# Kernel tuning notes

Hardware: AMD Instinct MI355X
Metric: run time of the kernel (lower is better)

Reference implementation:

```python
import jax, jax.numpy as jnp
import numpy as np

HEADS = 4
OUT = 64  # hidden_channels


def gat_conv(x, src, dst, N, W, att_src, att_dst, bias):
    # x: [N, Fin] -> h: [N, H, C]
    h = (x @ W).reshape(N, HEADS, OUT)
    a_s = (h * att_src).sum(-1)  # [N, H]
    a_d = (h * att_dst).sum(-1)  # [N, H]
    logits = jax.nn.leaky_relu(a_s[src] + a_d[dst], negative_slope=0.2)  # [E, H]
    # segment softmax over incoming edges of each destination node
    m = jax.ops.segment_max(logits, dst, num_segments=N)
    e = jnp.exp(logits - m[dst])
    z = jax.ops.segment_sum(e, dst, num_segments=N)
    alpha = e / (z[dst] + 1e-16)
    out = jax.ops.segment_sum(h[src] * alpha[:, :, None], dst, num_segments=N)
    return out.reshape(N, HEADS * OUT) + bias


def setup_inputs() -> dict:
    key = jax.random.key(0)
    ks = jax.random.split(key, 16)
    N, E, F = 50000, 800000, 128
    HC = HEADS * OUT  # 256
    s = 0.1
    return {
        "x": jax.random.normal(ks[0], (N, F), jnp.float32),
        "edge_index": jax.random.randint(ks[1], (2, E), 0, N, dtype=jnp.int32),
        "W1": jax.random.normal(ks[2], (F, HC), jnp.float32) * s,
        "as1": jax.random.normal(ks[3], (1, HEADS, OUT), jnp.float32) * s,
        "ad1": jax.random.normal(ks[4], (1, HEADS, OUT), jnp.float32) * s,
        "b1": jnp.zeros((HC,), jnp.float32),
        "W2": jax.random.normal(ks[5], (HC, HC), jnp.float32) * s,
        "as2": jax.random.normal(ks[6], (1, HEADS, OUT), jnp.float32) * s,
        "ad2": jax.random.normal(ks[7], (1, HEADS, OUT), jnp.float32) * s,
        "b2": jnp.zeros((HC,), jnp.float32),
        "lw1": jax.random.normal(ks[8], (HC, OUT), jnp.float32) * s,
        "lb1": jnp.zeros((OUT,), jnp.float32),
        "lw2": jax.random.normal(ks[9], (OUT, 2), jnp.float32) * s,
        "lb2": jnp.zeros((2,), jnp.float32),
    }


def reference(x, edge_index, W1, as1, ad1, b1, W2, as2, ad2, b2, lw1, lb1, lw2, lb2):
    N = x.shape[0]
    # PyG GATConv default add_self_loops=True
    loop = jnp.arange(N, dtype=edge_index.dtype)
    src = jnp.concatenate([edge_index[0], loop])
    dst = jnp.concatenate([edge_index[1], loop])
    h = jax.nn.elu(gat_conv(x, src, dst, N, W1, as1, ad1, b1))
    # dropout is identity at inference
    h = jax.nn.elu(gat_conv(h, src, dst, N, W2, as2, ad2, b2))
    h = jax.nn.relu(h @ lw1 + lb1)
    return jax.nn.log_softmax(h @ lw2 + lb2, axis=1)
```

## Files before the change

### kernel.cpp

```cpp
#include <hip/hip_runtime.h>
#include <math.h>


typedef __attribute__((ext_vector_type(8))) _Float16 half8v;
typedef __attribute__((ext_vector_type(4))) float f32x4;

__device__ __forceinline__ float lrelu(float x) { return x > 0.f ? x : 0.2f * x; }
__device__ __forceinline__ float elu1(float x) { return x > 0.f ? x : (__expf(x) - 1.f); }

__global__ void convert_x_kernel(const float* __restrict__ src, _Float16* __restrict__ dst,
                                 long n) {
  long i = ((long)blockIdx.x * blockDim.x + threadIdx.x) * 8;
  if (i >= n) return;
  float4 a = *(const float4*)(src + i);
  float4 b = *(const float4*)(src + i + 4);
  half8v o = {(_Float16)a.x, (_Float16)a.y, (_Float16)a.z, (_Float16)a.w,
              (_Float16)b.x, (_Float16)b.y, (_Float16)b.z, (_Float16)b.w};
  *(half8v*)(dst + i) = o;
}

__global__ void convert_weights_kernel(const float* __restrict__ W1, const float* __restrict__ W2,
                                       const float* __restrict__ lw1,
                                       _Float16* __restrict__ o1, _Float16* __restrict__ o2,
                                       _Float16* __restrict__ o3) {
  int t = blockIdx.x * blockDim.x + threadIdx.x;
  if (t < 32768) {
    int n = t >> 7, k = t & 127;
    o1[t] = (_Float16)W1[(long)k * 256 + n];
  } else if (t < 98304) {
    int i = t - 32768;
    int n = i >> 8, k = i & 255;
    o2[i] = (_Float16)W2[(long)k * 256 + n];
  } else if (t < 114688) {
    int i = t - 98304;
    int n = i >> 8, k = i & 255;
    o3[i] = (_Float16)lw1[(long)k * 64 + n];
  }
}

__global__ void zero_int_kernel(int* __restrict__ p, int n) {
  int i = blockIdx.x * blockDim.x + threadIdx.x;
  if (i < n) p[i] = 0;
}

__global__ void count_kernel(const int* __restrict__ dst, int E, int* __restrict__ indeg) {
  int e = blockIdx.x * blockDim.x + threadIdx.x;
  if (e < E) atomicAdd(&indeg[dst[e]], 1);
}

__global__ void scan_block_kernel(const int* __restrict__ in, int* __restrict__ incl,
                                  int* __restrict__ bsum, int N) {
  __shared__ int wsum[16];
  int gid = blockIdx.x * 1024 + threadIdx.x;
  int lane = threadIdx.x & 63, w = threadIdx.x >> 6;
  int v = (gid < N) ? in[gid] : 0;
  int sv = v;
#pragma unroll
  for (int o = 1; o < 64; o <<= 1) {
    int t = __shfl_up(sv, o);
    if (lane >= o) sv += t;
  }
  if (lane == 63) wsum[w] = sv;
  __syncthreads();
  if (w == 0) {
    int bs = (lane < 16) ? wsum[lane] : 0;
#pragma unroll
    for (int o = 1; o < 16; o <<= 1) {
      int t = __shfl_up(bs, o);
      if (lane >= o) bs += t;
    }
    if (lane < 16) wsum[lane] = bs;
  }
  __syncthreads();
  if (w > 0) sv += wsum[w - 1];
  if (gid < N) incl[gid] = sv;
  if (threadIdx.x == 1023) bsum[blockIdx.x] = sv;
}

__global__ void scan_tops_kernel(int* __restrict__ bsum, int nb) {
  int lane = threadIdx.x;
  int v = (lane < nb) ? bsum[lane] : 0;
#pragma unroll
  for (int o = 1; o < 64; o <<= 1) {
    int t = __shfl_up(v, o);
    if (lane >= o) v += t;
  }
  if (lane < nb) bsum[lane] = v;
}

__global__ void scan_finalize_kernel(const int* __restrict__ in, const int* __restrict__ incl,
                                     const int* __restrict__ bsum, int* __restrict__ off,
                                     int* __restrict__ cursor, int N) {
  int gid = blockIdx.x * blockDim.x + threadIdx.x;
  if (gid >= N) return;
  int b = gid >> 10;
  int ic = incl[gid] + ((b > 0) ? bsum[b - 1] : 0);
  off[gid + 1] = ic;
  cursor[gid] = ic - in[gid];
  if (gid == 0) off[0] = 0;
}

__global__ void fill_kernel(const int* __restrict__ src, const int* __restrict__ dst, int E,
                            int* __restrict__ cursor, int* __restrict__ csr_src,
                            int* __restrict__ csr_dst) {
  int e = blockIdx.x * blockDim.x + threadIdx.x;
  if (e < E) {
    int d = dst[e];
    int pos = atomicAdd(&cursor[d], 1);
    csr_src[pos] = src[e];
    csr_dst[pos] = d;
  }
}

__launch_bounds__(256)
__global__ void mfma_gemm_attn_kernel(const _Float16* __restrict__ A,
                                      const _Float16* __restrict__ B,
                                      const float* __restrict__ att_s,
                                      const float* __restrict__ att_d,
                                      _Float16* __restrict__ C,
                                      float* __restrict__ a_s, float* __restrict__ a_d,
                                      int M, int K) {
  __shared__ _Float16 As[64][40];
  __shared__ _Float16 Bs[64][40];
  int tid = threadIdx.x;
  int bm = blockIdx.y * 64, bn = blockIdx.x * 64;
  int lane = tid & 63, wave = tid >> 6;
  int srow = tid >> 2, sch = (tid & 3) * 8;
  const _Float16* Ap = A + (long)(bm + srow) * K + sch;
  const _Float16* Bp = B + (long)(bn + srow) * K + sch;
  int fm = lane & 15, fq = lane >> 4;
  f32x4 acc[4];
#pragma unroll
  for (int cb = 0; cb < 4; ++cb) acc[cb] = (f32x4){0.f, 0.f, 0.f, 0.f};
  for (int k0 = 0; k0 < K; k0 += 32) {
    uint4 va = *(const uint4*)(Ap + k0);
    uint4 vb = *(const uint4*)(Bp + k0);
    *(uint4*)&As[srow][sch] = va;
    *(uint4*)&Bs[srow][sch] = vb;
    __syncthreads();
    half8v ah = *(const half8v*)&As[wave * 16 + fm][fq * 8];
#pragma unroll
    for (int cb = 0; cb < 4; ++cb) {
      half8v bh = *(const half8v*)&Bs[cb * 16 + fm][fq * 8];
      acc[cb] = __builtin_amdgcn_mfma_f32_16x16x32_f16(ah, bh, acc[cb], 0, 0, 0);
    }
    __syncthreads();
  }
  int row0 = bm + wave * 16 + fq * 4;
  int headi = bn >> 6;
  float asv[4], adv[4];
#pragma unroll
  for (int cb = 0; cb < 4; ++cb) {
    int col = bn + cb * 16 + fm;
    asv[cb] = att_s[col];
    adv[cb] = att_d[col];
  }
#pragma unroll
  for (int r = 0; r < 4; ++r) {
    int row = row0 + r;
    float sp = 0.f, dp = 0.f;
#pragma unroll
    for (int cb = 0; cb < 4; ++cb) {
      float v = acc[cb][r];
      sp = fmaf(v, asv[cb], sp);
      dp = fmaf(v, adv[cb], dp);
      if (row < M) C[(long)row * 256 + bn + cb * 16 + fm] = (_Float16)v;
    }
#pragma unroll
    for (int o = 1; o < 16; o <<= 1) {
      sp += __shfl_xor(sp, o);
      dp += __shfl_xor(dp, o);
    }
    if (fm == 0 && row < M) {
      a_s[(long)row * 4 + headi] = sp;
      a_d[(long)row * 4 + headi] = dp;
    }
  }
}

__launch_bounds__(256)
__global__ void head_mfma_kernel(const _Float16* __restrict__ A, const _Float16* __restrict__ B,
                                 const float* __restrict__ lb1, const float* __restrict__ lw2,
                                 const float* __restrict__ lb2, float* __restrict__ out, int M) {
  __shared__ _Float16 As[64][40];
  __shared__ _Float16 Bs[64][40];
  int tid = threadIdx.x;
  int bm = blockIdx.x * 64;
  int lane = tid & 63, wave = tid >> 6;
  int srow = tid >> 2, sch = (tid & 3) * 8;
  const _Float16* Ap = A + (long)(bm + srow) * 256 + sch;
  const _Float16* Bp = B + (long)srow * 256 + sch;
  int fm = lane & 15, fq = lane >> 4;
  f32x4 acc[4];
#pragma unroll
  for (int cb = 0; cb < 4; ++cb) acc[cb] = (f32x4){0.f, 0.f, 0.f, 0.f};
  for (int k0 = 0; k0 < 256; k0 += 32) {
    uint4 va = *(const uint4*)(Ap + k0);
    uint4 vb = *(const uint4*)(Bp + k0);
    *(uint4*)&As[srow][sch] = va;
    *(uint4*)&Bs[srow][sch] = vb;
    __syncthreads();
    half8v ah = *(const half8v*)&As[wave * 16 + fm][fq * 8];
#pragma unroll
    for (int cb = 0; cb < 4; ++cb) {
      half8v bh = *(const half8v*)&Bs[cb * 16 + fm][fq * 8];
      acc[cb] = __builtin_amdgcn_mfma_f32_16x16x32_f16(ah, bh, acc[cb], 0, 0, 0);
    }
    __syncthreads();
  }
  float lb1c[4], w20[4], w21[4];
#pragma unroll
  for (int cb = 0; cb < 4; ++cb) {
    int col = cb * 16 + fm;
    lb1c[cb] = lb1[col];
    w20[cb] = lw2[col * 2 + 0];
    w21[cb] = lw2[col * 2 + 1];
  }
  float b20 = lb2[0], b21 = lb2[1];
#pragma unroll
  for (int r = 0; r < 4; ++r) {
    float v0 = 0.f, v1 = 0.f;
#pragma unroll
    for (int cb = 0; cb < 4; ++cb) {
      float s = fmaxf(acc[cb][r] + lb1c[cb], 0.f);
      v0 = fmaf(s, w20[cb], v0);
      v1 = fmaf(s, w21[cb], v1);
    }
#pragma unroll
    for (int o = 1; o < 16; o <<= 1) {
      v0 += __shfl_xor(v0, o);
      v1 += __shfl_xor(v1, o);
    }
    if (fm == 0) {
      int row = bm + wave * 16 + fq * 4 + r;
      if (row < M) {
        v0 += b20;
        v1 += b21;
        float mx = fmaxf(v0, v1);
        float ls = mx + logf(expf(v0 - mx) + expf(v1 - mx));
        out[(long)row * 2 + 0] = v0 - ls;
        out[(long)row * 2 + 1] = v1 - ls;
      }
    }
  }
}

__global__ void edge_logits_kernel(const int* __restrict__ csr_src, const int* __restrict__ csr_dst,
                                   const float* __restrict__ a_s, const float* __restrict__ a_d,
                                   float* __restrict__ logits, int E) {
  int e = blockIdx.x * blockDim.x + threadIdx.x;
  if (e >= E) return;
  int s = csr_src[e], d = csr_dst[e];
  float4 as4 = *(const float4*)(a_s + (long)s * 4);
  float4 ad4 = *(const float4*)(a_d + (long)d * 4);
  float4 o;
  o.x = lrelu(as4.x + ad4.x);
  o.y = lrelu(as4.y + ad4.y);
  o.z = lrelu(as4.z + ad4.z);
  o.w = lrelu(as4.w + ad4.w);
  *(float4*)(logits + (long)e * 4) = o;
}

__launch_bounds__(256)
__global__ void gat_aggregate4_kernel(const _Float16* __restrict__ h,
                                      const float* __restrict__ a_s,
                                      const float* __restrict__ a_d,
                                      const int* __restrict__ off,
                                      const int* __restrict__ csr_src,
                                      const float* __restrict__ logits,
                                      const float* __restrict__ bias,
                                      _Float16* __restrict__ outp, int N) {
  int wid = (blockIdx.x * blockDim.x + threadIdx.x) >> 6;
  int lane = threadIdx.x & 63;
  if (wid >= N) return;
  int c = lane & 31, hlf = lane >> 5, head4 = c >> 3;
  int h1 = lane & 3, sl1 = lane >> 2;
  int beg = off[wid], cnt = off[wid + 1] - beg;
  float self_l = lrelu(a_s[wid * 4 + h1] + a_d[wid * 4 + h1]);
  float m = self_l;
  for (int c0 = sl1; c0 < cnt; c0 += 16) m = fmaxf(m, logits[(long)(beg + c0) * 4 + h1]);
  m = fmaxf(m, __shfl_xor(m, 4));
  m = fmaxf(m, __shfl_xor(m, 8));
  m = fmaxf(m, __shfl_xor(m, 16));
  m = fmaxf(m, __shfl_xor(m, 32));
  float mh = __shfl(m, head4);
  float selfc = __shfl(self_l, head4);
  float acc[8] = {};
  float z = 0.f;
  if (hlf == 0) {
    z = __expf(selfc - mh);
    half8v sr = *(const half8v*)(h + (long)wid * 256 + c * 8);
#pragma unroll
    for (int i = 0; i < 8; ++i) acc[i] = z * (float)sr[i];
  }
  for (int c0 = 0; c0 < cnt; c0 += 16) {
    int i1 = c0 + sl1;
    float pv = (i1 < cnt) ? __expf(logits[(long)(beg + i1) * 4 + h1] - m) : 0.f;
    int i2 = c0 + (lane & 15);
    int sv = (i2 < cnt) ? csr_src[beg + i2] : 0;
#pragma unroll
    for (int j = 0; j < 16; j += 2) {
      if (c0 + j >= cnt) break;
      int e = j + hlf;
      int s = __shfl(sv, e);
      float p = __shfl(pv, e * 4 + head4);
      z += p;
      half8v rv = *(const half8v*)(h + (long)s * 256 + c * 8);
      acc[0] = fmaf(p, (float)rv[0], acc[0]);
      acc[1] = fmaf(p, (float)rv[1], acc[1]);
      acc[2] = fmaf(p, (float)rv[2], acc[2]);
      acc[3] = fmaf(p, (float)rv[3], acc[3]);
      acc[4] = fmaf(p, (float)rv[4], acc[4]);
      acc[5] = fmaf(p, (float)rv[5], acc[5]);
      acc[6] = fmaf(p, (float)rv[6], acc[6]);
      acc[7] = fmaf(p, (float)rv[7], acc[7]);
    }
  }
  z += __shfl_xor(z, 32);
#pragma unroll
  for (int i = 0; i < 8; ++i) acc[i] += __shfl_xor(acc[i], 32);
  if (hlf == 0) {
    float inv = 1.f / z;
    half8v o;
#pragma unroll
    for (int i = 0; i < 8; ++i) o[i] = (_Float16)elu1(fmaf(acc[i], inv, bias[c * 8 + i]));
    *(half8v*)(outp + (long)wid * 256 + c * 8) = o;
  }
}

static inline int cdiv(int a, int b) { return (a + b - 1) / b; }

extern "C" void kernel_launch(void* const* d_in, const int* in_sizes, int n_in,
                              void* d_out, int out_size, void* d_ws, size_t ws_size,
                              hipStream_t stream) {
  const float* x = (const float*)d_in[0];
  const int* ei = (const int*)d_in[1];
  const float* W1 = (const float*)d_in[2];
  const float* as1 = (const float*)d_in[3];
  const float* ad1 = (const float*)d_in[4];
  const float* b1 = (const float*)d_in[5];
  const float* W2 = (const float*)d_in[6];
  const float* as2 = (const float*)d_in[7];
  const float* ad2 = (const float*)d_in[8];
  const float* b2 = (const float*)d_in[9];
  const float* lw1 = (const float*)d_in[10];
  const float* lb1 = (const float*)d_in[11];
  const float* lw2 = (const float*)d_in[12];
  const float* lb2 = (const float*)d_in[13];
  float* out = (float*)d_out;

  int N = in_sizes[0] / 128;
  int E = in_sizes[1] / 2;
  int Mp = cdiv(N, 64) * 64;

  char* ws = (char*)d_ws;
  _Float16* A1 = (_Float16*)ws; ws += (size_t)Mp * 128 * 2;
  _Float16* Wt1 = (_Float16*)ws; ws += 256 * 128 * 2;
  _Float16* Wt2 = (_Float16*)ws; ws += 256 * 256 * 2;
  _Float16* WL = (_Float16*)ws; ws += 64 * 256 * 2;
  _Float16* C = (_Float16*)ws; ws += (size_t)Mp * 256 * 2;
  _Float16* h2 = (_Float16*)ws; ws += (size_t)Mp * 256 * 2;
  float* aS = (float*)ws; ws += (size_t)N * 4 * 4;
  float* aD = (float*)ws; ws += (size_t)N * 4 * 4;
  float* logits = (float*)ws; ws += (size_t)E * 4 * 4;
  int* csr_src = (int*)ws; ws += (size_t)E * 4;
  int* csr_dst = (int*)ws; ws += (size_t)E * 4;
  int* indeg = (int*)ws; ws += (size_t)N * 4;
  int* cursor = (int*)ws; ws += (size_t)N * 4;
  int* off = (int*)ws; ws += (size_t)(N + 4) * 4;
  int* incl = (int*)ws; ws += (size_t)N * 4;
  int* bsum = (int*)ws; ws += 64 * 4;

  const int* e_src = ei;
  const int* e_dst = ei + E;
  int nb = cdiv(N, 1024);

  convert_x_kernel<<<cdiv(N * 128 / 8, 256), 256, 0, stream>>>(x, A1, (long)N * 128);
  convert_weights_kernel<<<cdiv(114688, 256), 256, 0, stream>>>(W1, W2, lw1, Wt1, Wt2, WL);

  zero_int_kernel<<<cdiv(N, 256), 256, 0, stream>>>(indeg, N);
  count_kernel<<<cdiv(E, 256), 256, 0, stream>>>(e_dst, E, indeg);
  scan_block_kernel<<<nb, 1024, 0, stream>>>(indeg, incl, bsum, N);
  scan_tops_kernel<<<1, 64, 0, stream>>>(bsum, nb);
  scan_finalize_kernel<<<cdiv(N, 256), 256, 0, stream>>>(indeg, incl, bsum, off, cursor, N);
  fill_kernel<<<cdiv(E, 256), 256, 0, stream>>>(e_src, e_dst, E, cursor, csr_src, csr_dst);

  mfma_gemm_attn_kernel<<<dim3(4, Mp / 64), 256, 0, stream>>>(A1, Wt1, as1, ad1, C, aS, aD, N, 128);
  edge_logits_kernel<<<cdiv(E, 256), 256, 0, stream>>>(csr_src, csr_dst, aS, aD, logits, E);
  gat_aggregate4_kernel<<<cdiv(N, 4), 256, 0, stream>>>(C, aS, aD, off, csr_src, logits, b1, h2, N);

  mfma_gemm_attn_kernel<<<dim3(4, Mp / 64), 256, 0, stream>>>(h2, Wt2, as2, ad2, C, aS, aD, N, 256);
  edge_logits_kernel<<<cdiv(E, 256), 256, 0, stream>>>(csr_src, csr_dst, aS, aD, logits, E);
  gat_aggregate4_kernel<<<cdiv(N, 4), 256, 0, stream>>>(C, aS, aD, off, csr_src, logits, b2, h2, N);

  head_mfma_kernel<<<Mp / 64, 256, 0, stream>>>(h2, WL, lb1, lw2, lb2, out, N);
}
```

Measured before the change: 389.3 us.

## Fuse x conversion into GEMM, compute edge logits inline, drop scan-tops kernel

Result: faster. 377.4 us (-3.1%).

```diff
diff --git a/kernel.cpp b/kernel.cpp
--- a/kernel.cpp
+++ b/kernel.cpp
@@ -7,17 +7,6 @@
 
 __device__ __forceinline__ float lrelu(float x) { return x > 0.f ? x : 0.2f * x; }
 __device__ __forceinline__ float elu1(float x) { return x > 0.f ? x : (__expf(x) - 1.f); }
-
-__global__ void convert_x_kernel(const float* __restrict__ src, _Float16* __restrict__ dst,
-                                 long n) {
-  long i = ((long)blockIdx.x * blockDim.x + threadIdx.x) * 8;
-  if (i >= n) return;
-  float4 a = *(const float4*)(src + i);
-  float4 b = *(const float4*)(src + i + 4);
-  half8v o = {(_Float16)a.x, (_Float16)a.y, (_Float16)a.z, (_Float16)a.w,
-              (_Float16)b.x, (_Float16)b.y, (_Float16)b.z, (_Float16)b.w};
-  *(half8v*)(dst + i) = o;
-}
 
 __global__ void convert_weights_kernel(const float* __restrict__ W1, const float* __restrict__ W2,
                                        const float* __restrict__ lw1,
@@ -77,43 +66,32 @@
   if (threadIdx.x == 1023) bsum[blockIdx.x] = sv;
 }
 
-__global__ void scan_tops_kernel(int* __restrict__ bsum, int nb) {
-  int lane = threadIdx.x;
-  int v = (lane < nb) ? bsum[lane] : 0;
-#pragma unroll
-  for (int o = 1; o < 64; o <<= 1) {
-    int t = __shfl_up(v, o);
-    if (lane >= o) v += t;
-  }
-  if (lane < nb) bsum[lane] = v;
-}
-
 __global__ void scan_finalize_kernel(const int* __restrict__ in, const int* __restrict__ incl,
                                      const int* __restrict__ bsum, int* __restrict__ off,
                                      int* __restrict__ cursor, int N) {
   int gid = blockIdx.x * blockDim.x + threadIdx.x;
   if (gid >= N) return;
   int b = gid >> 10;
-  int ic = incl[gid] + ((b > 0) ? bsum[b - 1] : 0);
+  int carry = 0;
+  for (int k = 0; k < b; ++k) carry += bsum[k];
+  int ic = incl[gid] + carry;
   off[gid + 1] = ic;
   cursor[gid] = ic - in[gid];
   if (gid == 0) off[0] = 0;
 }
 
 __global__ void fill_kernel(const int* __restrict__ src, const int* __restrict__ dst, int E,
-                            int* __restrict__ cursor, int* __restrict__ csr_src,
-                            int* __restrict__ csr_dst) {
+                            int* __restrict__ cursor, int* __restrict__ csr_src) {
   int e = blockIdx.x * blockDim.x + threadIdx.x;
   if (e < E) {
-    int d = dst[e];
-    int pos = atomicAdd(&cursor[d], 1);
+    int pos = atomicAdd(&cursor[dst[e]], 1);
     csr_src[pos] = src[e];
-    csr_dst[pos] = d;
-  }
-}
-
+  }
+}
+
+template <typename AT>
 __launch_bounds__(256)
-__global__ void mfma_gemm_attn_kernel(const _Float16* __restrict__ A,
+__global__ void mfma_gemm_attn_kernel(const AT* __restrict__ A,
                                       const _Float16* __restrict__ B,
                                       const float* __restrict__ att_s,
                                       const float* __restrict__ att_d,
@@ -126,16 +104,27 @@
   int bm = blockIdx.y * 64, bn = blockIdx.x * 64;
   int lane = tid & 63, wave = tid >> 6;
   int srow = tid >> 2, sch = (tid & 3) * 8;
-  const _Float16* Ap = A + (long)(bm + srow) * K + sch;
+  const AT* Ap = A + (long)(bm + srow) * K + sch;
   const _Float16* Bp = B + (long)(bn + srow) * K + sch;
+  bool arow_ok = (bm + srow) < M;
   int fm = lane & 15, fq = lane >> 4;
   f32x4 acc[4];
 #pragma unroll
   for (int cb = 0; cb < 4; ++cb) acc[cb] = (f32x4){0.f, 0.f, 0.f, 0.f};
   for (int k0 = 0; k0 < K; k0 += 32) {
-    uint4 va = *(const uint4*)(Ap + k0);
+    half8v a8 = {0, 0, 0, 0, 0, 0, 0, 0};
+    if (arow_ok) {
+      if constexpr (sizeof(AT) == 4) {
+        float4 f0 = *(const float4*)(Ap + k0);
+        float4 f1 = *(const float4*)(Ap + k0 + 4);
+        a8 = (half8v){(_Float16)f0.x, (_Float16)f0.y, (_Float16)f0.z, (_Float16)f0.w,
+                      (_Float16)f1.x, (_Float16)f1.y, (_Float16)f1.z, (_Float16)f1.w};
+      } else {
+        a8 = *(const half8v*)(Ap + k0);
+      }
+    }
     uint4 vb = *(const uint4*)(Bp + k0);
-    *(uint4*)&As[srow][sch] = va;
+    *(half8v*)&As[srow][sch] = a8;
     *(uint4*)&Bs[srow][sch] = vb;
     __syncthreads();
     half8v ah = *(const half8v*)&As[wave * 16 + fm][fq * 8];
@@ -245,29 +234,12 @@
   }
 }
 
-__global__ void edge_logits_kernel(const int* __restrict__ csr_src, const int* __restrict__ csr_dst,
-                                   const float* __restrict__ a_s, const float* __restrict__ a_d,
-                                   float* __restrict__ logits, int E) {
-  int e = blockIdx.x * blockDim.x + threadIdx.x;
-  if (e >= E) return;
-  int s = csr_src[e], d = csr_dst[e];
-  float4 as4 = *(const float4*)(a_s + (long)s * 4);
-  float4 ad4 = *(const float4*)(a_d + (long)d * 4);
-  float4 o;
-  o.x = lrelu(as4.x + ad4.x);
-  o.y = lrelu(as4.y + ad4.y);
-  o.z = lrelu(as4.z + ad4.z);
-  o.w = lrelu(as4.w + ad4.w);
-  *(float4*)(logits + (long)e * 4) = o;
-}
-
 __launch_bounds__(256)
-__global__ void gat_aggregate4_kernel(const _Float16* __restrict__ h,
+__global__ void gat_aggregate5_kernel(const _Float16* __restrict__ h,
                                       const float* __restrict__ a_s,
                                       const float* __restrict__ a_d,
                                       const int* __restrict__ off,
                                       const int* __restrict__ csr_src,
-                                      const float* __restrict__ logits,
                                       const float* __restrict__ bias,
                                       _Float16* __restrict__ outp, int N) {
   int wid = (blockIdx.x * blockDim.x + threadIdx.x) >> 6;
@@ -276,9 +248,13 @@
   int c = lane & 31, hlf = lane >> 5, head4 = c >> 3;
   int h1 = lane & 3, sl1 = lane >> 2;
   int beg = off[wid], cnt = off[wid + 1] - beg;
-  float self_l = lrelu(a_s[wid * 4 + h1] + a_d[wid * 4 + h1]);
+  float ad_h1 = a_d[wid * 4 + h1];
+  float self_l = lrelu(a_s[wid * 4 + h1] + ad_h1);
   float m = self_l;
-  for (int c0 = sl1; c0 < cnt; c0 += 16) m = fmaxf(m, logits[(long)(beg + c0) * 4 + h1]);
+  for (int c0 = sl1; c0 < cnt; c0 += 16) {
+    int s = csr_src[beg + c0];
+    m = fmaxf(m, lrelu(a_s[(long)s * 4 + h1] + ad_h1));
+  }
   m = fmaxf(m, __shfl_xor(m, 4));
   m = fmaxf(m, __shfl_xor(m, 8));
   m = fmaxf(m, __shfl_xor(m, 16));
@@ -294,10 +270,12 @@
     for (int i = 0; i < 8; ++i) acc[i] = z * (float)sr[i];
   }
   for (int c0 = 0; c0 < cnt; c0 += 16) {
-    int i1 = c0 + sl1;
-    float pv = (i1 < cnt) ? __expf(logits[(long)(beg + i1) * 4 + h1] - m) : 0.f;
     int i2 = c0 + (lane & 15);
     int sv = (i2 < cnt) ? csr_src[beg + i2] : 0;
+    int i1 = c0 + sl1;
+    int sp = __shfl(sv, sl1);
+    float pv = 0.f;
+    if (i1 < cnt) pv = __expf(lrelu(a_s[(long)sp * 4 + h1] + ad_h1) - m);
 #pragma unroll
     for (int j = 0; j < 16; j += 2) {
       if (c0 + j >= cnt) break;
@@ -354,7 +332,6 @@
   int Mp = cdiv(N, 64) * 64;
 
   char* ws = (char*)d_ws;
-  _Float16* A1 = (_Float16*)ws; ws += (size_t)Mp * 128 * 2;
   _Float16* Wt1 = (_Float16*)ws; ws += 256 * 128 * 2;
   _Float16* Wt2 = (_Float16*)ws; ws += 256 * 256 * 2;
   _Float16* WL = (_Float16*)ws; ws += 64 * 256 * 2;
@@ -362,9 +339,7 @@
   _Float16* h2 = (_Float16*)ws; ws += (size_t)Mp * 256 * 2;
   float* aS = (float*)ws; ws += (size_t)N * 4 * 4;
   float* aD = (float*)ws; ws += (size_t)N * 4 * 4;
-  float* logits = (float*)ws; ws += (size_t)E * 4 * 4;
   int* csr_src = (int*)ws; ws += (size_t)E * 4;
-  int* csr_dst = (int*)ws; ws += (size_t)E * 4;
   int* indeg = (int*)ws; ws += (size_t)N * 4;
   int* cursor = (int*)ws; ws += (size_t)N * 4;
   int* off = (int*)ws; ws += (size_t)(N + 4) * 4;
@@ -375,23 +350,21 @@
   const int* e_dst = ei + E;
   int nb = cdiv(N, 1024);
 
-  convert_x_kernel<<<cdiv(N * 128 / 8, 256), 256, 0, stream>>>(x, A1, (long)N * 128);
   convert_weights_kernel<<<cdiv(114688, 256), 256, 0, stream>>>(W1, W2, lw1, Wt1, Wt2, WL);
 
   zero_int_kernel<<<cdiv(N, 256), 256, 0, stream>>>(indeg, N);
   count_kernel<<<cdiv(E, 256), 256, 0, stream>>>(e_dst, E, indeg);
   scan_block_kernel<<<nb, 1024, 0, stream>>>(indeg, incl, bsum, N);
-  scan_tops_kernel<<<1, 64, 0, stream>>>(bsum, nb);
   scan_finalize_kernel<<<cdiv(N, 256), 256, 0, stream>>>(indeg, incl, bsum, off, cursor, N);
-  fill_kernel<<<cdiv(E, 256), 256, 0, stream>>>(e_src, e_dst, E, cursor, csr_src, csr_dst);
-
-  mfma_gemm_attn_kernel<<<dim3(4, Mp / 64), 256, 0, stream>>>(A1, Wt1, as1, ad1, C, aS, aD, N, 128);
-  edge_logits_kernel<<<cdiv(E, 256), 256, 0, stream>>>(csr_src, csr_dst, aS, aD, logits, E);
-  gat_aggregate4_kernel<<<cdiv(N, 4), 256, 0, stream>>>(C, aS, aD, off, csr_src, logits, b1, h2, N);
-
-  mfma_gemm_attn_kernel<<<dim3(4, Mp / 64), 256, 0, stream>>>(h2, Wt2, as2, ad2, C, aS, aD, N, 256);
-  edge_logits_kernel<<<cdiv(E, 256), 256, 0, stream>>>(csr_src, csr_dst, aS, aD, logits, E);
-  gat_aggregate4_kernel<<<cdiv(N, 4), 256, 0, stream>>>(C, aS, aD, off, csr_src, logits, b2, h2, N);
+  fill_kernel<<<cdiv(E, 256), 256, 0, stream>>>(e_src, e_dst, E, cursor, csr_src);
+
+  mfma_gemm_attn_kernel<float><<<dim3(4, Mp / 64), 256, 0, stream>>>(x, Wt1, as1, ad1, C, aS, aD,
+                                                                     N, 128);
+  gat_aggregate5_kernel<<<cdiv(N, 4), 256, 0, stream>>>(C, aS, aD, off, csr_src, b1, h2, N);
+
+  mfma_gemm_attn_kernel<_Float16><<<dim3(4, Mp / 64), 256, 0, stream>>>(h2, Wt2, as2, ad2, C, aS,
+                                                                        aD, N, 256);
+  gat_aggregate5_kernel<<<cdiv(N, 4), 256, 0, stream>>>(C, aS, aD, off, csr_src, b2, h2, N);
 
   head_mfma_kernel<<<Mp / 64, 256, 0, stream>>>(h2, WL, lb1, lw2, lb2, out, N);
 }
```
